# Performance work log

Measured on AMD Instinct MI355X. Metric: run time of the kernel, lower is better.

The kernel has to match this reference:

```python
import jax, jax.numpy as jnp
import numpy as np

BATCH, SEQ, DIM, NH = 2, 4096, 1024, 16
HD = DIM // NH
BLOCK = 64


def setup_inputs() -> dict:
    key = jax.random.key(0)
    ks = jax.random.split(key, 8)
    x = jax.random.normal(ks[0], (BATCH, SEQ, DIM), dtype=jnp.float32)
    # standard RoPE tables: (seq, head_dim)
    inv_freq = 1.0 / (10000.0 ** (jnp.arange(0, HD, 2, dtype=jnp.float32) / HD))
    t = jnp.arange(SEQ, dtype=jnp.float32)
    freqs = jnp.outer(t, inv_freq)                      # (SEQ, HD//2)
    emb = jnp.concatenate([freqs, freqs], axis=-1)      # (SEQ, HD)
    cos, sin = jnp.cos(emb), jnp.sin(emb)
    s = 0.02
    wq = jax.random.normal(ks[1], (DIM, DIM), jnp.float32) * s
    wk = jax.random.normal(ks[2], (DIM, DIM), jnp.float32) * s
    wv = jax.random.normal(ks[3], (DIM, DIM), jnp.float32) * s
    wo = jax.random.normal(ks[4], (DIM, DIM), jnp.float32) * s
    A_log = jax.random.normal(ks[5], (NH,), jnp.float32) * 0.1
    w_dt_w = jax.random.normal(ks[6], (DIM, NH), jnp.float32) * s
    w_dt_b = jnp.zeros((NH,), jnp.float32)
    return {"x": x, "cos": cos, "sin": sin, "wq": wq, "wk": wk, "wv": wv,
            "wo": wo, "A_log": A_log, "w_dt_w": w_dt_w, "w_dt_b": w_dt_b}


def segsum(a):
    """a: (..., T) -> (..., T, T) lower-triangular segment sums, -inf above diag."""
    T = a.shape[-1]
    cs = jnp.cumsum(a, axis=-1)
    seg = cs[..., :, None] - cs[..., None, :]
    mask = jnp.tril(jnp.ones((T, T), dtype=bool))
    return jnp.where(mask, seg, -jnp.inf)


def rotate_half(t):
    t1, t2 = jnp.split(t, 2, axis=-1)
    return jnp.concatenate([-t2, t1], axis=-1)


def ssd(X, A, B, C, block_len):
    """Mamba-2 SSD chunked scan.
    X: (b,l,h,p)  A: (b,l,h)  B,C: (b,l,h,n)
    """
    b, l, h, p = X.shape
    c = l // block_len
    Xc = X.reshape(b, c, block_len, h, p)
    Bc = B.reshape(b, c, block_len, h, -1)
    Cc = C.reshape(b, c, block_len, h, -1)
    Ac = jnp.transpose(A.reshape(b, c, block_len, h), (0, 3, 1, 2))  # (b,h,c,l)
    A_cumsum = jnp.cumsum(Ac, axis=-1)
    # intra-chunk (diagonal block) output
    L = jnp.exp(segsum(Ac))                                          # (b,h,c,l,l)
    Y_diag = jnp.einsum('bclhn,bcshn,bhcls,bcshp->bclhp', Cc, Bc, L, Xc)
    # per-chunk states
    decay_states = jnp.exp(A_cumsum[:, :, :, -1:] - A_cumsum)        # (b,h,c,l)
    states = jnp.einsum('bclhn,bhcl,bclhp->bchpn', Bc, decay_states, Xc)
    init = jnp.zeros_like(states[:, :1])
    states = jnp.concatenate([init, states], axis=1)                 # (b,c+1,h,p,n)
    # inter-chunk recurrence (done as a 1-SS matmul over chunk axis)
    A_last = jnp.pad(A_cumsum[:, :, :, -1], ((0, 0), (0, 0), (1, 0)))
    decay_chunk = jnp.exp(segsum(A_last))                            # (b,h,c+1,c+1)
    new_states = jnp.einsum('bhzc,bchpn->bzhpn', decay_chunk, states)
    states, final_state = new_states[:, :-1], new_states[:, -1]
    # state -> output contribution
    state_decay_out = jnp.exp(A_cumsum)
    Y_off = jnp.einsum('bclhn,bchpn,bhcl->bclhp', Cc, states, state_decay_out)
    Y = (Y_diag + Y_off).reshape(b, l, h, p)
    return Y, final_state


def reference(x, cos, sin, wq, wk, wv, wo, A_log, w_dt_w, w_dt_b):
    b, l, dim = x.shape
    h = A_log.shape[0]
    d = dim // h
    xq = (x @ wq).reshape(b, l, h, d)
    xk = (x @ wk).reshape(b, l, h, d)
    xv = (x @ wv).reshape(b, l, h, d)
    cb = cos[None, :, None, :]
    sb = sin[None, :, None, :]
    xq = xq * cb + rotate_half(xq) * sb
    xk = xk * cb + rotate_half(xk) * sb
    dt = jax.nn.softplus(x @ w_dt_w + w_dt_b)           # (b,l,h)
    A = -jnp.exp(A_log)[None, None, :] * dt             # (b,l,h)
    X = xv * dt[..., None]                              # (b,l,h,d)
    Y, state = ssd(X, A, xk, xq, BLOCK)
    # replicate torch's transpose(1,2).view(b, l, -1) exactly:
    y = jnp.transpose(Y, (0, 2, 1, 3)).reshape(b, l, h * d)
    return y @ wo, state
```

## Files before the change

### kernel.cpp

```cpp
#include <hip/hip_runtime.h>


typedef __bf16 bf16x8 __attribute__((ext_vector_type(8)));
typedef float f32x4 __attribute__((ext_vector_type(4)));
typedef unsigned int u32x4 __attribute__((ext_vector_type(4)));
typedef unsigned short u16x8 __attribute__((ext_vector_type(8)));
typedef unsigned short u16x4 __attribute__((ext_vector_type(4)));

__device__ __forceinline__ unsigned short f2bf(float f) {
  unsigned int u = __builtin_bit_cast(unsigned int, f);
  u += 0x7fffu + ((u >> 16) & 1u);
  return (unsigned short)(u >> 16);
}
__device__ __forceinline__ float bf2f(unsigned short s) {
  unsigned int u = ((unsigned int)s) << 16;
  return __builtin_bit_cast(float, u);
}

#define GLOAD16(gp, lp)                                                \
  __builtin_amdgcn_global_load_lds(                                    \
      (const __attribute__((address_space(1))) void*)(gp),             \
      (__attribute__((address_space(3))) void*)(lp), 16, 0, 0)

__global__ __launch_bounds__(256) void convert_bf16_kernel(
    const float* __restrict__ in, unsigned short* __restrict__ out, int n4,
    const float* __restrict__ wdt, unsigned short* __restrict__ wdt_bf) {
  const int bx = blockIdx.x;
  if (bx < 8192) {
    int g = bx * 256 + threadIdx.x;
    if (g < n4) {
      f32x4 v = *reinterpret_cast<const f32x4*>(in + (size_t)g * 4);
      u16x4 o;
      o.x = f2bf(v.x); o.y = f2bf(v.y); o.z = f2bf(v.z); o.w = f2bf(v.w);
      *reinterpret_cast<u16x4*>(out + (size_t)g * 4) = o;
    }
  } else {
    const int g = (bx - 8192) * 256 + threadIdx.x;
    const int n = g >> 10, k = g & 1023;
    wdt_bf[g] = f2bf(wdt[k * 16 + n]);
  }
}

__global__ __launch_bounds__(256) void transpose_w_kernel(
    const float* __restrict__ w0, const float* __restrict__ w1,
    const float* __restrict__ w2, const float* __restrict__ w3,
    unsigned short* __restrict__ wt) {
  __shared__ float tile[32][33];
  const int z = blockIdx.z;
  const float* w = (z == 0) ? w0 : (z == 1) ? w1 : (z == 2) ? w2 : w3;
  unsigned short* o = wt + (size_t)z * 1024 * 1024;
  const int bx = blockIdx.x, by = blockIdx.y;
  const int tx = threadIdx.x, ty = threadIdx.y;
#pragma unroll
  for (int i = 0; i < 4; ++i)
    tile[ty + i * 8][tx] = w[(size_t)(by * 32 + ty + i * 8) * 1024 + bx * 32 + tx];
  __syncthreads();
#pragma unroll
  for (int i = 0; i < 4; ++i)
    o[(size_t)(bx * 32 + ty + i * 8) * 1024 + by * 32 + tx] = f2bf(tile[tx][ty + i * 8]);
}

__global__ __launch_bounds__(256) void dt_gemm_kernel(
    const unsigned short* __restrict__ A,
    const unsigned short* __restrict__ Bt,
    const float* __restrict__ bdt, float* __restrict__ dt) {
  __shared__ unsigned short As[2 * 64 * 32];
  const int tid = threadIdx.x, lane = tid & 63, w = tid >> 6;
  const int m0 = blockIdx.x * 64;
  const unsigned short* ga =
      A + (size_t)(m0 + w * 16 + (lane >> 2)) * 1024 + (lane & 3) * 8;
  unsigned short* la = As + w * 512;
  const int lr = lane & 15, lk = (lane >> 4) * 8;
  const unsigned short* gb = Bt + (size_t)lr * 1024 + lk;
  f32x4 acc = {};
  for (int kt = 0; kt < 1024; kt += 64) {
    GLOAD16(ga + kt, la);
    GLOAD16(ga + kt + 32, la + 2048);
    bf16x8 bF0 = *reinterpret_cast<const bf16x8*>(gb + kt);
    bf16x8 bF1 = *reinterpret_cast<const bf16x8*>(gb + kt + 32);
    __syncthreads();
    bf16x8 aF0 = *reinterpret_cast<const bf16x8*>(&As[(w * 16 + lr) * 32 + lk]);
    bf16x8 aF1 = *reinterpret_cast<const bf16x8*>(&As[2048 + (w * 16 + lr) * 32 + lk]);
    acc = __builtin_amdgcn_mfma_f32_16x16x32_bf16(aF0, bF0, acc, 0, 0, 0);
    acc = __builtin_amdgcn_mfma_f32_16x16x32_bf16(aF1, bF1, acc, 0, 0, 0);
    __syncthreads();
  }
  const int h = lr;
  const float bv = bdt[h];
#pragma unroll
  for (int r = 0; r < 4; ++r) {
    const int row = m0 + w * 16 + (lane >> 4) * 4 + r;
    const float a = acc[r] + bv;
    const float sp = (a > 0.f) ? (a + log1pf(expf(-a))) : log1pf(expf(a));
    dt[(size_t)row * 16 + h] = sp;
  }
}

template <int EPI>
__global__ __launch_bounds__(256) void gemm128_kernel(
    const unsigned short* __restrict__ A, const unsigned short* __restrict__ Bt,
    void* __restrict__ out0, unsigned short* __restrict__ out1,
    unsigned short* __restrict__ out2, const float* __restrict__ cosb,
    const float* __restrict__ sinb, const float* __restrict__ dtb) {
  __shared__ unsigned short As[128 * 64];
  __shared__ unsigned short Bs[128 * 64];
  const int tid = threadIdx.x, lane = tid & 63, w = tid >> 6;
  const int m0 = blockIdx.y * 128, n0 = blockIdx.x * 128;
  const int rw = lane >> 3;
  const int cu = ((lane & 7) ^ rw) * 8;
  const unsigned short* ga = A + (size_t)(m0 + w * 8 + rw) * 1024 + cu;
  const unsigned short* gb = Bt + (size_t)(n0 + w * 8 + rw) * 1024 + cu;
  unsigned short* la = As + (w * 8) * 64;
  unsigned short* lb = Bs + (w * 8) * 64;
  const int lr = lane & 15, lku = lane >> 4;
  const int wr = w >> 1, wc = w & 1;
  const int xr = lr & 7;
  f32x4 acc[4][4] = {};
  for (int kt = 0; kt < 1024; kt += 64) {
#pragma unroll
    for (int g = 0; g < 4; ++g) {
      GLOAD16(ga + kt + (size_t)(g * 32) * 1024, la + g * 32 * 64);
      GLOAD16(gb + kt + (size_t)(g * 32) * 1024, lb + g * 32 * 64);
    }
    __syncthreads();
#pragma unroll
    for (int kk = 0; kk < 2; ++kk) {
      const int un = (kk * 4 + lku) ^ xr;
      bf16x8 aF[4], bF[4];
#pragma unroll
      for (int i = 0; i < 4; ++i) {
        aF[i] = *reinterpret_cast<const bf16x8*>(&As[(wr * 64 + i * 16 + lr) * 64 + un * 8]);
        bF[i] = *reinterpret_cast<const bf16x8*>(&Bs[(wc * 64 + i * 16 + lr) * 64 + un * 8]);
      }
#pragma unroll
      for (int i = 0; i < 4; ++i)
#pragma unroll
        for (int j = 0; j < 4; ++j)
          acc[i][j] = __builtin_amdgcn_mfma_f32_16x16x32_bf16(aF[i], bF[j], acc[i][j], 0, 0, 0);
    }
    __syncthreads();
  }
  const int r0 = m0 + wr * 64 + ((lane >> 4) << 2);
  if constexpr (EPI == 0) {
    float* O = (float*)out0;
    const int c0 = n0 + wc * 64 + lr;
#pragma unroll
    for (int i = 0; i < 4; ++i)
#pragma unroll
      for (int j = 0; j < 4; ++j)
#pragma unroll
        for (int r = 0; r < 4; ++r)
          O[(size_t)(r0 + i * 16 + r) * 1024 + c0 + j * 16] = acc[i][j][r];
  } else {
    const int col = n0 + wc * 64;
    if (col < 2048) {
      unsigned short* O = (col < 1024) ? (unsigned short*)out0 : out1;
      const int cbase = col & 1023;
#pragma unroll
      for (int i = 0; i < 4; ++i)
#pragma unroll
        for (int jj = 0; jj < 2; ++jj) {
          const int d1 = jj * 16 + lr;
#pragma unroll
          for (int r = 0; r < 4; ++r) {
            const int row = r0 + i * 16 + r;
            const int l = row & 4095;
            const float cv = cosb[(size_t)l * 64 + d1];
            const float sv = sinb[(size_t)l * 64 + d1];
            const float v1 = acc[i][jj][r], v2 = acc[i][jj + 2][r];
            O[(size_t)row * 1024 + cbase + jj * 16 + lr] = f2bf(v1 * cv - v2 * sv);
            O[(size_t)row * 1024 + cbase + jj * 16 + lr + 32] = f2bf(v2 * cv + v1 * sv);
          }
        }
    } else {
      unsigned short* O = out2;
      const int cbase = col - 2048;
      const int h = cbase >> 6;
#pragma unroll
      for (int i = 0; i < 4; ++i)
#pragma unroll
        for (int r = 0; r < 4; ++r) {
          const int row = r0 + i * 16 + r;
          const float dtv = dtb[(size_t)row * 16 + h];
#pragma unroll
          for (int j = 0; j < 4; ++j)
            O[(size_t)row * 1024 + cbase + j * 16 + lr] = f2bf(acc[i][j][r] * dtv);
        }
    }
  }
}

__global__ __launch_bounds__(256) void ssd_states_kernel(
    const unsigned short* __restrict__ Kb, const unsigned short* __restrict__ Xb,
    const float* __restrict__ dtb, const float* __restrict__ A_log,
    unsigned short* __restrict__ chunk_states, float* __restrict__ chunk_dec) {
  __shared__ unsigned short T1[64 * 72], T2[64 * 72];
  __shared__ unsigned short BtL[64 * 72], XdL[64 * 72];
  __shared__ float csL[64], decL[64];
  const int c = blockIdx.x, h = blockIdx.y, b = blockIdx.z;
  const int tid = threadIdx.x, lane = tid & 63, w = tid >> 6;
  const size_t gbase = ((size_t)(b * 4096 + c * 64)) * 1024 + h * 64;
  {
    const int s = tid >> 2, e0 = (tid & 3) * 16;
    const unsigned short* gk = Kb + gbase + (size_t)s * 1024 + e0;
    const unsigned short* gx = Xb + gbase + (size_t)s * 1024 + e0;
    *(u32x4*)&T1[s * 72 + e0] = *(const u32x4*)gk;
    *(u32x4*)&T1[s * 72 + e0 + 8] = *(const u32x4*)(gk + 8);
    *(u32x4*)&T2[s * 72 + e0] = *(const u32x4*)gx;
    *(u32x4*)&T2[s * 72 + e0 + 8] = *(const u32x4*)(gx + 8);
  }
  if (w == 0) {
    float a = -expf(A_log[h]) * dtb[((size_t)(b * 4096 + c * 64 + lane)) * 16 + h];
    float v = a;
#pragma unroll
    for (int d = 1; d < 64; d <<= 1) {
      float o = __shfl_up(v, d, 64);
      if (lane >= d) v += o;
    }
    const float tot = __shfl(v, 63, 64);
    csL[lane] = v;
    decL[lane] = expf(tot - v);
    if (lane == 0) chunk_dec[((size_t)(b * 16 + h)) * 64 + c] = expf(tot);
  }
  __syncthreads();
#pragma unroll
  for (int q = 0; q < 2; ++q) {
    const int p = lane;
    const int s0 = (q * 4 + w) * 8;
    u16x8 vb, vx;
#pragma unroll
    for (int j = 0; j < 8; ++j) {
      vb[j] = T1[(s0 + j) * 72 + p];
      vx[j] = f2bf(bf2f(T2[(s0 + j) * 72 + p]) * decL[s0 + j]);
    }
    *(u16x8*)&BtL[p * 72 + s0] = vb;
    *(u16x8*)&XdL[p * 72 + s0] = vx;
  }
  __syncthreads();
  const int lr = lane & 15, lk = (lane >> 4) * 8;
  f32x4 acc[4] = {};
#pragma unroll
  for (int kt = 0; kt < 64; kt += 32) {
    bf16x8 aF = *reinterpret_cast<const bf16x8*>(&XdL[(w * 16 + lr) * 72 + kt + lk]);
#pragma unroll
    for (int j = 0; j < 4; ++j) {
      bf16x8 bF = *reinterpret_cast<const bf16x8*>(&BtL[(j * 16 + lr) * 72 + kt + lk]);
      acc[j] = __builtin_amdgcn_mfma_f32_16x16x32_bf16(aF, bF, acc[j], 0, 0, 0);
    }
  }
  const size_t stb = ((size_t)((b * 64 + c) * 16 + h)) * 4096;
#pragma unroll
  for (int j = 0; j < 4; ++j)
#pragma unroll
    for (int r = 0; r < 4; ++r)
      chunk_states[stb + (size_t)(w * 16 + (lane >> 4) * 4 + r) * 64 + j * 16 + lr] =
          f2bf(acc[j][r]);
}

__global__ __launch_bounds__(256) void scan_kernel(
    const unsigned short* __restrict__ chunk_states, const float* __restrict__ chunk_dec,
    unsigned short* __restrict__ inc_bf, float* __restrict__ state_out) {
  __shared__ float decs[64];
  const int g = blockIdx.x * 256 + threadIdx.x;
  const int n = g & 63, p = (g >> 6) & 63, h = (g >> 12) & 15, b = g >> 16;
  if (threadIdx.x < 64)
    decs[threadIdx.x] = chunk_dec[(size_t)((blockIdx.x * 256) >> 12 & 15) * 64 +
                                  (size_t)(blockIdx.x >> 8) * 1024 + threadIdx.x];
  __syncthreads();
  const size_t pn = (size_t)p * 64 + n;
  const size_t stride = (size_t)16 * 4096;
  const size_t base0 = ((size_t)(b * 64) * 16 + h) * 4096 + pn;
  float inc = 0.f;
  float cur = bf2f(chunk_states[base0]);
  for (int c = 0; c < 64; ++c) {
    const size_t idx = base0 + (size_t)c * stride;
    inc_bf[idx] = f2bf(inc);
    float nxt = (c < 63) ? bf2f(chunk_states[idx + stride]) : 0.f;
    inc = decs[c] * inc + cur;
    cur = nxt;
  }
  state_out[((size_t)(b * 16 + h) * 64 + p) * 64 + n] = inc;
}

__global__ __launch_bounds__(256) void ssd_y_kernel(
    const unsigned short* __restrict__ Qb, const unsigned short* __restrict__ Kb,
    const unsigned short* __restrict__ Xb, const unsigned short* __restrict__ Sg,
    const float* __restrict__ dtb, const float* __restrict__ A_log,
    unsigned short* __restrict__ y_bf) {
  __shared__ unsigned short Cb[64 * 72], Bb[64 * 72], Sb[64 * 72];
  __shared__ unsigned short Xt[64 * 72], TG[64 * 72];
  __shared__ float csL[64], sdeL[64];
  const int c = blockIdx.x, h = blockIdx.y, b = blockIdx.z;
  const int tid = threadIdx.x, lane = tid & 63, w = tid >> 6;
  const size_t gbase = ((size_t)(b * 4096 + c * 64)) * 1024 + h * 64;
  const size_t sbase = ((size_t)((b * 64 + c) * 16 + h)) * 4096;
  {
    const int s = tid >> 2, e0 = (tid & 3) * 16;
    const unsigned short* gq = Qb + gbase + (size_t)s * 1024 + e0;
    const unsigned short* gk = Kb + gbase + (size_t)s * 1024 + e0;
    const unsigned short* gx = Xb + gbase + (size_t)s * 1024 + e0;
    const unsigned short* gs = Sg + sbase + (size_t)s * 64 + e0;
    *(u32x4*)&Cb[s * 72 + e0] = *(const u32x4*)gq;
    *(u32x4*)&Cb[s * 72 + e0 + 8] = *(const u32x4*)(gq + 8);
    *(u32x4*)&Bb[s * 72 + e0] = *(const u32x4*)gk;
    *(u32x4*)&Bb[s * 72 + e0 + 8] = *(const u32x4*)(gk + 8);
    *(u32x4*)&TG[s * 72 + e0] = *(const u32x4*)gx;
    *(u32x4*)&TG[s * 72 + e0 + 8] = *(const u32x4*)(gx + 8);
    *(u32x4*)&Sb[s * 72 + e0] = *(const u32x4*)gs;
    *(u32x4*)&Sb[s * 72 + e0 + 8] = *(const u32x4*)(gs + 8);
  }
  if (w == 0) {
    float a = -expf(A_log[h]) * dtb[((size_t)(b * 4096 + c * 64 + lane)) * 16 + h];
    float v = a;
#pragma unroll
    for (int d = 1; d < 64; d <<= 1) {
      float o = __shfl_up(v, d, 64);
      if (lane >= d) v += o;
    }
    csL[lane] = v;
    sdeL[lane] = expf(v);
  }
  __syncthreads();
  const int lr = lane & 15, lk = (lane >> 4) * 8;
  f32x4 g[4] = {};
#pragma unroll
  for (int kt = 0; kt < 64; kt += 32) {
    bf16x8 aF = *reinterpret_cast<const bf16x8*>(&Cb[(w * 16 + lr) * 72 + kt + lk]);
#pragma unroll
    for (int j = 0; j < 4; ++j) {
      bf16x8 bF = *reinterpret_cast<const bf16x8*>(&Bb[(j * 16 + lr) * 72 + kt + lk]);
      g[j] = __builtin_amdgcn_mfma_f32_16x16x32_bf16(aF, bF, g[j], 0, 0, 0);
    }
  }
#pragma unroll
  for (int q = 0; q < 2; ++q) {
    const int p = lane;
    const int s0 = (q * 4 + w) * 8;
    u16x8 vx;
#pragma unroll
    for (int j = 0; j < 8; ++j) vx[j] = TG[(s0 + j) * 72 + p];
    *(u16x8*)&Xt[p * 72 + s0] = vx;
  }
  __syncthreads();
#pragma unroll
  for (int j = 0; j < 4; ++j)
#pragma unroll
    for (int r = 0; r < 4; ++r) {
      const int l = w * 16 + (lane >> 4) * 4 + r;
      const int s = j * 16 + lr;
      const float gm = (l >= s) ? g[j][r] * expf(csL[l] - csL[s]) : 0.f;
      TG[l * 72 + s] = f2bf(gm);
    }
  {
    const int rl = tid >> 2, e0 = (tid & 3) * 16;
    const float sde = sdeL[rl];
#pragma unroll
    for (int half = 0; half < 2; ++half) {
      u16x8 v = *(u16x8*)&Cb[rl * 72 + e0 + half * 8];
#pragma unroll
      for (int j = 0; j < 8; ++j) v[j] = f2bf(bf2f(v[j]) * sde);
      *(u16x8*)&Cb[rl * 72 + e0 + half * 8] = v;
    }
  }
  __syncthreads();
  f32x4 acc[4] = {};
#pragma unroll
  for (int kt = 0; kt < 64; kt += 32) {
    bf16x8 aG = *reinterpret_cast<const bf16x8*>(&TG[(w * 16 + lr) * 72 + kt + lk]);
    bf16x8 aC = *reinterpret_cast<const bf16x8*>(&Cb[(w * 16 + lr) * 72 + kt + lk]);
#pragma unroll
    for (int j = 0; j < 4; ++j) {
      bf16x8 bX = *reinterpret_cast<const bf16x8*>(&Xt[(j * 16 + lr) * 72 + kt + lk]);
      bf16x8 bS = *reinterpret_cast<const bf16x8*>(&Sb[(j * 16 + lr) * 72 + kt + lk]);
      acc[j] = __builtin_amdgcn_mfma_f32_16x16x32_bf16(aG, bX, acc[j], 0, 0, 0);
      acc[j] = __builtin_amdgcn_mfma_f32_16x16x32_bf16(aC, bS, acc[j], 0, 0, 0);
    }
  }
  const size_t orow = (size_t)b * 4096 + h * 256 + c * 4 + w;
#pragma unroll
  for (int j = 0; j < 4; ++j)
#pragma unroll
    for (int r = 0; r < 4; ++r) {
      const int li = (lane >> 4) * 4 + r;
      y_bf[orow * 1024 + li * 64 + j * 16 + lr] = f2bf(acc[j][r]);
    }
}

extern "C" void kernel_launch(void* const* d_in, const int* in_sizes, int n_in,
                              void* d_out, int out_size, void* d_ws, size_t ws_size,
                              hipStream_t stream) {
  (void)in_sizes; (void)n_in; (void)out_size; (void)ws_size;
  const float* x = (const float*)d_in[0];
  const float* cosb = (const float*)d_in[1];
  const float* sinb = (const float*)d_in[2];
  const float* wq = (const float*)d_in[3];
  const float* wk = (const float*)d_in[4];
  const float* wv = (const float*)d_in[5];
  const float* wo = (const float*)d_in[6];
  const float* A_log = (const float*)d_in[7];
  const float* wdt = (const float*)d_in[8];
  const float* bdt = (const float*)d_in[9];

  float* out_y = (float*)d_out;
  float* out_state = out_y + 8388608;

  const size_t MBB = 1048576;
  char* ws = (char*)d_ws;
  unsigned short* x_bf = (unsigned short*)(ws);
  unsigned short* w_t = (unsigned short*)(ws + 16 * MBB);
  unsigned short* q_bf = (unsigned short*)(ws + 24 * MBB);
  unsigned short* k_bf = (unsigned short*)(ws + 40 * MBB);
  unsigned short* xv_bf = (unsigned short*)(ws + 56 * MBB);
  float* dtb = (float*)(ws + 72 * MBB);
  unsigned short* wdt_bf = (unsigned short*)(ws + 73 * MBB);
  unsigned short* chunk_states = (unsigned short*)(ws + 74 * MBB);
  float* chunk_dec = (float*)(ws + 90 * MBB);
  unsigned short* inc_bf = (unsigned short*)(ws + 91 * MBB);

  convert_bf16_kernel<<<8256, 256, 0, stream>>>(x, x_bf, 2097152, wdt, wdt_bf);
  transpose_w_kernel<<<dim3(32, 32, 4), dim3(32, 8), 0, stream>>>(wq, wk, wv, wo, w_t);
  dt_gemm_kernel<<<128, 256, 0, stream>>>(x_bf, wdt_bf, bdt, dtb);

  gemm128_kernel<3><<<dim3(24, 64), 256, 0, stream>>>(
      x_bf, w_t, q_bf, k_bf, xv_bf, cosb, sinb, dtb);

  ssd_states_kernel<<<dim3(64, 16, 2), 256, 0, stream>>>(k_bf, xv_bf, dtb, A_log,
                                                         chunk_states, chunk_dec);
  scan_kernel<<<512, 256, 0, stream>>>(chunk_states, chunk_dec, inc_bf, out_state);
  ssd_y_kernel<<<dim3(64, 16, 2), 256, 0, stream>>>(q_bf, k_bf, xv_bf, inc_bf, dtb, A_log,
                                                    x_bf );

  gemm128_kernel<0><<<dim3(8, 64), 256, 0, stream>>>(
      x_bf , w_t + 3 * MBB, out_y, nullptr, nullptr, nullptr, nullptr, nullptr);
}
```

Measured before the change: 162.4 us.

## Use 256x128 GEMM tiles with 512 threads and triple-buffered async LDS loads

Replaces the 128x128 single-buffered GEMM with a 256x128 tile run by 8 waves. It uses a three-stage ring of LDS buffers filled by global_load_lds, with vmcnt-based waits and one barrier per k-step. MFMA blocks are raised with s_setprio. The goal is to overlap global loads with matrix math and raise per-wave reuse, at the cost of much more LDS (144 KB), fewer blocks and a different wave-to-column mapping in the RoPE and dt epilogues.

```diff
diff --git a/kernel.cpp b/kernel.cpp
--- a/kernel.cpp
+++ b/kernel.cpp
@@ -97,94 +97,124 @@
 }
 
 template <int EPI>
-__global__ __launch_bounds__(256) void gemm128_kernel(
+__global__ __launch_bounds__(512, 2) void gemm256_kernel(
     const unsigned short* __restrict__ A, const unsigned short* __restrict__ Bt,
     void* __restrict__ out0, unsigned short* __restrict__ out1,
     unsigned short* __restrict__ out2, const float* __restrict__ cosb,
     const float* __restrict__ sinb, const float* __restrict__ dtb) {
-  __shared__ unsigned short As[128 * 64];
-  __shared__ unsigned short Bs[128 * 64];
+  __shared__ unsigned short AsBuf[3][256 * 64];
+  __shared__ unsigned short BsBuf[3][128 * 64];
   const int tid = threadIdx.x, lane = tid & 63, w = tid >> 6;
-  const int m0 = blockIdx.y * 128, n0 = blockIdx.x * 128;
-  const int rw = lane >> 3;
-  const int cu = ((lane & 7) ^ rw) * 8;
-  const unsigned short* ga = A + (size_t)(m0 + w * 8 + rw) * 1024 + cu;
-  const unsigned short* gb = Bt + (size_t)(n0 + w * 8 + rw) * 1024 + cu;
-  unsigned short* la = As + (w * 8) * 64;
-  unsigned short* lb = Bs + (w * 8) * 64;
-  const int lr = lane & 15, lku = lane >> 4;
-  const int wr = w >> 1, wc = w & 1;
+  const int wr = w >> 2, wc = w & 3;
+  const int m0 = blockIdx.y * 256, n0 = blockIdx.x * 128;
+  const int srw = lane >> 3;
+  const int scu = ((lane & 7) ^ srw) * 8;
+  const unsigned short* gA = A + (size_t)(m0 + w * 32 + srw) * 1024 + scu;
+  const unsigned short* gB = Bt + (size_t)(n0 + w * 16 + srw) * 1024 + scu;
+  const int lr = lane & 15, l4 = lane >> 4;
   const int xr = lr & 7;
-  f32x4 acc[4][4] = {};
-  for (int kt = 0; kt < 1024; kt += 64) {
-#pragma unroll
-    for (int g = 0; g < 4; ++g) {
-      GLOAD16(ga + kt + (size_t)(g * 32) * 1024, la + g * 32 * 64);
-      GLOAD16(gb + kt + (size_t)(g * 32) * 1024, lb + g * 32 * 64);
-    }
-    __syncthreads();
+  f32x4 acc[8][2] = {};
+
+  auto STAGE = [&](unsigned short* as, unsigned short* bs, int kt) {
+#pragma unroll
+    for (int g = 0; g < 4; ++g)
+      GLOAD16(gA + kt + (size_t)(g * 8) * 1024, as + (w * 32 + g * 8) * 64);
+#pragma unroll
+    for (int g = 0; g < 2; ++g)
+      GLOAD16(gB + kt + (size_t)(g * 8) * 1024, bs + (w * 16 + g * 8) * 64);
+  };
+  auto COMPUTE = [&](const unsigned short* as, const unsigned short* bs) {
+    bf16x8 aF[2][8], bF[2][2];
 #pragma unroll
     for (int kk = 0; kk < 2; ++kk) {
-      const int un = (kk * 4 + lku) ^ xr;
-      bf16x8 aF[4], bF[4];
-#pragma unroll
-      for (int i = 0; i < 4; ++i) {
-        aF[i] = *reinterpret_cast<const bf16x8*>(&As[(wr * 64 + i * 16 + lr) * 64 + un * 8]);
-        bF[i] = *reinterpret_cast<const bf16x8*>(&Bs[(wc * 64 + i * 16 + lr) * 64 + un * 8]);
-      }
-#pragma unroll
-      for (int i = 0; i < 4; ++i)
-#pragma unroll
-        for (int j = 0; j < 4; ++j)
-          acc[i][j] = __builtin_amdgcn_mfma_f32_16x16x32_bf16(aF[i], bF[j], acc[i][j], 0, 0, 0);
-    }
-    __syncthreads();
-  }
-  const int r0 = m0 + wr * 64 + ((lane >> 4) << 2);
+      const int un = (((kk * 4 + l4) ^ xr) * 8);
+#pragma unroll
+      for (int i = 0; i < 8; ++i)
+        aF[kk][i] = *reinterpret_cast<const bf16x8*>(
+            &as[(wr * 128 + i * 16 + lr) * 64 + un]);
+#pragma unroll
+      for (int j = 0; j < 2; ++j)
+        bF[kk][j] = *reinterpret_cast<const bf16x8*>(
+            &bs[((wc >> 1) * 64 + (wc & 1) * 16 + j * 32 + lr) * 64 + un]);
+    }
+    __builtin_amdgcn_s_setprio(1);
+#pragma unroll
+    for (int kk = 0; kk < 2; ++kk)
+#pragma unroll
+      for (int i = 0; i < 8; ++i)
+#pragma unroll
+        for (int j = 0; j < 2; ++j)
+          acc[i][j] = __builtin_amdgcn_mfma_f32_16x16x32_bf16(
+              aF[kk][i], bF[kk][j], acc[i][j], 0, 0, 0);
+    __builtin_amdgcn_s_setprio(0);
+  };
+
+  unsigned short *pa0 = AsBuf[0], *pa1 = AsBuf[1], *pa2 = AsBuf[2];
+  unsigned short *pb0 = BsBuf[0], *pb1 = BsBuf[1], *pb2 = BsBuf[2];
+  STAGE(pa0, pb0, 0);
+  STAGE(pa1, pb1, 64);
+  asm volatile("s_waitcnt vmcnt(6)" ::: "memory");
+  __builtin_amdgcn_s_barrier();
+  asm volatile("" ::: "memory");
+  const int NT = 16;
+  for (int t = 0; t < NT; ++t) {
+    if (t < NT - 2) STAGE(pa2, pb2, (t + 2) * 64);
+    COMPUTE(pa0, pb0);
+    if (t < NT - 1) {
+      if (t < NT - 2)
+        asm volatile("s_waitcnt vmcnt(6)" ::: "memory");
+      else
+        asm volatile("s_waitcnt vmcnt(0)" ::: "memory");
+      __builtin_amdgcn_s_barrier();
+      asm volatile("" ::: "memory");
+    }
+    unsigned short* ta = pa0; pa0 = pa1; pa1 = pa2; pa2 = ta;
+    unsigned short* tb = pb0; pb0 = pb1; pb1 = pb2; pb2 = tb;
+  }
+
+  const int rbase = m0 + wr * 128 + l4 * 4;
   if constexpr (EPI == 0) {
     float* O = (float*)out0;
-    const int c0 = n0 + wc * 64 + lr;
-#pragma unroll
-    for (int i = 0; i < 4; ++i)
-#pragma unroll
-      for (int j = 0; j < 4; ++j)
+#pragma unroll
+    for (int i = 0; i < 8; ++i)
+#pragma unroll
+      for (int j = 0; j < 2; ++j) {
+        const int c = n0 + (wc >> 1) * 64 + (wc & 1) * 16 + j * 32 + lr;
 #pragma unroll
         for (int r = 0; r < 4; ++r)
-          O[(size_t)(r0 + i * 16 + r) * 1024 + c0 + j * 16] = acc[i][j][r];
+          O[(size_t)(rbase + i * 16 + r) * 1024 + c] = acc[i][j][r];
+      }
   } else {
-    const int col = n0 + wc * 64;
-    if (col < 2048) {
-      unsigned short* O = (col < 1024) ? (unsigned short*)out0 : out1;
-      const int cbase = col & 1023;
-#pragma unroll
-      for (int i = 0; i < 4; ++i)
-#pragma unroll
-        for (int jj = 0; jj < 2; ++jj) {
-          const int d1 = jj * 16 + lr;
-#pragma unroll
-          for (int r = 0; r < 4; ++r) {
-            const int row = r0 + i * 16 + r;
-            const int l = row & 4095;
-            const float cv = cosb[(size_t)l * 64 + d1];
-            const float sv = sinb[(size_t)l * 64 + d1];
-            const float v1 = acc[i][jj][r], v2 = acc[i][jj + 2][r];
-            O[(size_t)row * 1024 + cbase + jj * 16 + lr] = f2bf(v1 * cv - v2 * sv);
-            O[(size_t)row * 1024 + cbase + jj * 16 + lr + 32] = f2bf(v2 * cv + v1 * sv);
-          }
+    const int colh = n0 + (wc >> 1) * 64;
+    if (colh < 2048) {
+      unsigned short* O = (colh < 1024) ? (unsigned short*)out0 : out1;
+      const int cb = colh & 1023;
+      const int d1 = (wc & 1) * 16 + lr;
+#pragma unroll
+      for (int i = 0; i < 8; ++i)
+#pragma unroll
+        for (int r = 0; r < 4; ++r) {
+          const int row = rbase + i * 16 + r;
+          const int l = row & 4095;
+          const float cv = cosb[(size_t)l * 64 + d1];
+          const float sv = sinb[(size_t)l * 64 + d1];
+          const float v1 = acc[i][0][r], v2 = acc[i][1][r];
+          O[(size_t)row * 1024 + cb + d1] = f2bf(v1 * cv - v2 * sv);
+          O[(size_t)row * 1024 + cb + d1 + 32] = f2bf(v2 * cv + v1 * sv);
         }
     } else {
       unsigned short* O = out2;
-      const int cbase = col - 2048;
-      const int h = cbase >> 6;
-#pragma unroll
-      for (int i = 0; i < 4; ++i)
+      const int h = (colh - 2048) >> 6;
+      const int cb = colh - 2048 + (wc & 1) * 16;
+#pragma unroll
+      for (int i = 0; i < 8; ++i)
 #pragma unroll
         for (int r = 0; r < 4; ++r) {
-          const int row = r0 + i * 16 + r;
+          const int row = rbase + i * 16 + r;
           const float dtv = dtb[(size_t)row * 16 + h];
 #pragma unroll
-          for (int j = 0; j < 4; ++j)
-            O[(size_t)row * 1024 + cbase + j * 16 + lr] = f2bf(acc[i][j][r] * dtv);
+          for (int j = 0; j < 2; ++j)
+            O[(size_t)row * 1024 + cb + j * 32 + lr] = f2bf(acc[i][j][r] * dtv);
         }
     }
   }
@@ -421,7 +451,7 @@
   transpose_w_kernel<<<dim3(32, 32, 4), dim3(32, 8), 0, stream>>>(wq, wk, wv, wo, w_t);
   dt_gemm_kernel<<<128, 256, 0, stream>>>(x_bf, wdt_bf, bdt, dtb);
 
-  gemm128_kernel<3><<<dim3(24, 64), 256, 0, stream>>>(
+  gemm256_kernel<3><<<dim3(24, 32), 512, 0, stream>>>(
       x_bf, w_t, q_bf, k_bf, xv_bf, cosb, sinb, dtb);
 
   ssd_states_kernel<<<dim3(64, 16, 2), 256, 0, stream>>>(k_bf, xv_bf, dtb, A_log,
@@ -430,6 +460,6 @@
   ssd_y_kernel<<<dim3(64, 16, 2), 256, 0, stream>>>(q_bf, k_bf, xv_bf, inc_bf, dtb, A_log,
                                                     x_bf );
 
-  gemm128_kernel<0><<<dim3(8, 64), 256, 0, stream>>>(
+  gemm256_kernel<0><<<dim3(8, 32), 512, 0, stream>>>(
       x_bf , w_t + 3 * MBB, out_y, nullptr, nullptr, nullptr, nullptr, nullptr);
 }
```

After: 178.8 us. 1.1x slower.

## Replace QKV GEMM with 256x256 triple-buffered pipelined 8-wave kernel

Applied to the files above, without the earlier changes.

The fused QKV projection moves from a 128x128 tile with single-buffered LDS and full syncs to a 256x256 tile run by 512 threads. It uses a three-stage LDS ring with global_load_lds prefetch, split barriers, and setprio around the MFMA bursts so loads overlap compute. The larger tile raises reuse per LDS load but halves the K-step to 32 and cuts the grid from 1536 to 384 blocks. That can hurt CU fill on a large GPU and adds register pressure from 32 accumulators. The output projection is split into its own kernel, with no speed change intended there.

```diff
diff --git a/kernel.cpp b/kernel.cpp
--- a/kernel.cpp
+++ b/kernel.cpp
@@ -21,6 +21,13 @@
   __builtin_amdgcn_global_load_lds(                                    \
       (const __attribute__((address_space(1))) void*)(gp),             \
       (__attribute__((address_space(3))) void*)(lp), 16, 0, 0)
+
+#define BARR()                              \
+  do {                                      \
+    asm volatile("" ::: "memory");          \
+    __builtin_amdgcn_s_barrier();           \
+    asm volatile("" ::: "memory");          \
+  } while (0)
 
 __global__ __launch_bounds__(256) void convert_bf16_kernel(
     const float* __restrict__ in, unsigned short* __restrict__ out, int n4,
@@ -96,12 +103,129 @@
   }
 }
 
-template <int EPI>
-__global__ __launch_bounds__(256) void gemm128_kernel(
+__global__ __launch_bounds__(512, 2) void gemm256_qkv_kernel(
     const unsigned short* __restrict__ A, const unsigned short* __restrict__ Bt,
-    void* __restrict__ out0, unsigned short* __restrict__ out1,
-    unsigned short* __restrict__ out2, const float* __restrict__ cosb,
+    unsigned short* __restrict__ oq, unsigned short* __restrict__ ok,
+    unsigned short* __restrict__ ov, const float* __restrict__ cosb,
     const float* __restrict__ sinb, const float* __restrict__ dtb) {
+  __shared__ unsigned short As[3][8192];
+  __shared__ unsigned short Bs[3][8192];
+  const int tid = threadIdx.x, lane = tid & 63, w = tid >> 6;
+  const int wr = w >> 2, wc = w & 3;
+  const int m0 = blockIdx.y * 256, n0 = blockIdx.x * 256;
+  const int srow = lane >> 2;
+  const int sunit = (lane & 3) ^ (srow & 3);
+  const unsigned short* gA = A + (size_t)(m0 + w * 32 + srow) * 1024 + sunit * 8;
+  const unsigned short* gB = Bt + (size_t)(n0 + w * 32 + srow) * 1024 + sunit * 8;
+  const int lr = lane & 15, s4 = lane >> 4;
+  const int un = (s4 ^ (lr & 3)) * 8;
+  f32x4 acc[8][4] = {};
+
+  auto SA = [&](unsigned short* buf, int kt) {
+    GLOAD16(gA + kt, buf + w * 1024);
+    GLOAD16(gA + kt + (size_t)16 * 1024, buf + w * 1024 + 512);
+  };
+  auto SB = [&](unsigned short* buf, int kt) {
+    GLOAD16(gB + kt, buf + w * 1024);
+    GLOAD16(gB + kt + (size_t)16 * 1024, buf + w * 1024 + 512);
+  };
+
+  unsigned short *a0 = As[0], *a1 = As[1], *a2 = As[2];
+  unsigned short *b0 = Bs[0], *b1 = Bs[1], *b2 = Bs[2];
+  SA(a0, 0); SB(b0, 0);
+  SA(a1, 32); SB(b1, 32);
+  asm volatile("s_waitcnt vmcnt(4)" ::: "memory");
+  __builtin_amdgcn_s_barrier();
+
+  for (int t = 0; t < 32; ++t) {
+    const int kt2 = t * 32 + 64;
+    bf16x8 aF[4], bF[4];
+#pragma unroll
+    for (int i = 0; i < 4; ++i)
+      aF[i] = *reinterpret_cast<const bf16x8*>(
+          &a0[(wr * 128 + i * 16 + lr) * 32 + un]);
+#pragma unroll
+    for (int j = 0; j < 4; ++j)
+      bF[j] = *reinterpret_cast<const bf16x8*>(
+          &b0[(wc * 64 + j * 16 + lr) * 32 + un]);
+    if (t < 30) SA(a2, kt2);
+    BARR();
+    __builtin_amdgcn_sched_barrier(0);
+    __builtin_amdgcn_s_setprio(1);
+#pragma unroll
+    for (int i = 0; i < 4; ++i)
+#pragma unroll
+      for (int j = 0; j < 4; ++j)
+        acc[i][j] = __builtin_amdgcn_mfma_f32_16x16x32_bf16(
+            aF[i], bF[j], acc[i][j], 0, 0, 0);
+    __builtin_amdgcn_s_setprio(0);
+    BARR();
+    bf16x8 aG[4];
+#pragma unroll
+    for (int i = 0; i < 4; ++i)
+      aG[i] = *reinterpret_cast<const bf16x8*>(
+          &a0[(wr * 128 + (i + 4) * 16 + lr) * 32 + un]);
+    if (t < 30) SB(b2, kt2);
+    BARR();
+    __builtin_amdgcn_sched_barrier(0);
+    __builtin_amdgcn_s_setprio(1);
+#pragma unroll
+    for (int i = 0; i < 4; ++i)
+#pragma unroll
+      for (int j = 0; j < 4; ++j)
+        acc[i + 4][j] = __builtin_amdgcn_mfma_f32_16x16x32_bf16(
+            aG[i], bF[j], acc[i + 4][j], 0, 0, 0);
+    __builtin_amdgcn_s_setprio(0);
+    if (t < 30)
+      asm volatile("s_waitcnt vmcnt(4)" ::: "memory");
+    else if (t == 30)
+      asm volatile("s_waitcnt vmcnt(0)" ::: "memory");
+    if (t < 31) BARR();
+    unsigned short* ta = a0; a0 = a1; a1 = a2; a2 = ta;
+    unsigned short* tb = b0; b0 = b1; b1 = b2; b2 = tb;
+  }
+
+  const int rbase = m0 + wr * 128 + s4 * 4;
+  const int cblock = n0 + wc * 64;
+  if (cblock < 2048) {
+    unsigned short* O = (cblock < 1024) ? oq : ok;
+    const int cb = cblock & 1023;
+#pragma unroll
+    for (int i = 0; i < 8; ++i)
+#pragma unroll
+      for (int jj = 0; jj < 2; ++jj) {
+        const int d1 = jj * 16 + lr;
+#pragma unroll
+        for (int r = 0; r < 4; ++r) {
+          const int row = rbase + i * 16 + r;
+          const int l = row & 4095;
+          const float cv = cosb[(size_t)l * 64 + d1];
+          const float sv = sinb[(size_t)l * 64 + d1];
+          const float v1 = acc[i][jj][r], v2 = acc[i][jj + 2][r];
+          O[(size_t)row * 1024 + cb + d1] = f2bf(v1 * cv - v2 * sv);
+          O[(size_t)row * 1024 + cb + d1 + 32] = f2bf(v2 * cv + v1 * sv);
+        }
+      }
+  } else {
+    unsigned short* O = ov;
+    const int cb = cblock - 2048;
+    const int h = cb >> 6;
+#pragma unroll
+    for (int i = 0; i < 8; ++i)
+#pragma unroll
+      for (int r = 0; r < 4; ++r) {
+        const int row = rbase + i * 16 + r;
+        const float dtv = dtb[(size_t)row * 16 + h];
+#pragma unroll
+        for (int j = 0; j < 4; ++j)
+          O[(size_t)row * 1024 + cb + j * 16 + lr] = f2bf(acc[i][j][r] * dtv);
+      }
+  }
+}
+
+__global__ __launch_bounds__(256) void gemm128_wo_kernel(
+    const unsigned short* __restrict__ A, const unsigned short* __restrict__ Bt,
+    float* __restrict__ O) {
   __shared__ unsigned short As[128 * 64];
   __shared__ unsigned short Bs[128 * 64];
   const int tid = threadIdx.x, lane = tid & 63, w = tid >> 6;
@@ -125,12 +249,12 @@
     __syncthreads();
 #pragma unroll
     for (int kk = 0; kk < 2; ++kk) {
-      const int un = (kk * 4 + lku) ^ xr;
+      const int un = (((kk * 4 + lku) ^ xr) * 8);
       bf16x8 aF[4], bF[4];
 #pragma unroll
       for (int i = 0; i < 4; ++i) {
-        aF[i] = *reinterpret_cast<const bf16x8*>(&As[(wr * 64 + i * 16 + lr) * 64 + un * 8]);
-        bF[i] = *reinterpret_cast<const bf16x8*>(&Bs[(wc * 64 + i * 16 + lr) * 64 + un * 8]);
+        aF[i] = *reinterpret_cast<const bf16x8*>(&As[(wr * 64 + i * 16 + lr) * 64 + un]);
+        bF[i] = *reinterpret_cast<const bf16x8*>(&Bs[(wc * 64 + i * 16 + lr) * 64 + un]);
       }
 #pragma unroll
       for (int i = 0; i < 4; ++i)
@@ -141,53 +265,14 @@
     __syncthreads();
   }
   const int r0 = m0 + wr * 64 + ((lane >> 4) << 2);
-  if constexpr (EPI == 0) {
-    float* O = (float*)out0;
-    const int c0 = n0 + wc * 64 + lr;
-#pragma unroll
-    for (int i = 0; i < 4; ++i)
-#pragma unroll
-      for (int j = 0; j < 4; ++j)
-#pragma unroll
-        for (int r = 0; r < 4; ++r)
-          O[(size_t)(r0 + i * 16 + r) * 1024 + c0 + j * 16] = acc[i][j][r];
-  } else {
-    const int col = n0 + wc * 64;
-    if (col < 2048) {
-      unsigned short* O = (col < 1024) ? (unsigned short*)out0 : out1;
-      const int cbase = col & 1023;
-#pragma unroll
-      for (int i = 0; i < 4; ++i)
-#pragma unroll
-        for (int jj = 0; jj < 2; ++jj) {
-          const int d1 = jj * 16 + lr;
-#pragma unroll
-          for (int r = 0; r < 4; ++r) {
-            const int row = r0 + i * 16 + r;
-            const int l = row & 4095;
-            const float cv = cosb[(size_t)l * 64 + d1];
-            const float sv = sinb[(size_t)l * 64 + d1];
-            const float v1 = acc[i][jj][r], v2 = acc[i][jj + 2][r];
-            O[(size_t)row * 1024 + cbase + jj * 16 + lr] = f2bf(v1 * cv - v2 * sv);
-            O[(size_t)row * 1024 + cbase + jj * 16 + lr + 32] = f2bf(v2 * cv + v1 * sv);
-          }
-        }
-    } else {
-      unsigned short* O = out2;
-      const int cbase = col - 2048;
-      const int h = cbase >> 6;
-#pragma unroll
-      for (int i = 0; i < 4; ++i)
-#pragma unroll
-        for (int r = 0; r < 4; ++r) {
-          const int row = r0 + i * 16 + r;
-          const float dtv = dtb[(size_t)row * 16 + h];
-#pragma unroll
-          for (int j = 0; j < 4; ++j)
-            O[(size_t)row * 1024 + cbase + j * 16 + lr] = f2bf(acc[i][j][r] * dtv);
-        }
-    }
-  }
+  const int c0 = n0 + wc * 64 + lr;
+#pragma unroll
+  for (int i = 0; i < 4; ++i)
+#pragma unroll
+    for (int j = 0; j < 4; ++j)
+#pragma unroll
+      for (int r = 0; r < 4; ++r)
+        O[(size_t)(r0 + i * 16 + r) * 1024 + c0 + j * 16] = acc[i][j][r];
 }
 
 __global__ __launch_bounds__(256) void ssd_states_kernel(
@@ -421,7 +506,7 @@
   transpose_w_kernel<<<dim3(32, 32, 4), dim3(32, 8), 0, stream>>>(wq, wk, wv, wo, w_t);
   dt_gemm_kernel<<<128, 256, 0, stream>>>(x_bf, wdt_bf, bdt, dtb);
 
-  gemm128_kernel<3><<<dim3(24, 64), 256, 0, stream>>>(
+  gemm256_qkv_kernel<<<dim3(12, 32), 512, 0, stream>>>(
       x_bf, w_t, q_bf, k_bf, xv_bf, cosb, sinb, dtb);
 
   ssd_states_kernel<<<dim3(64, 16, 2), 256, 0, stream>>>(k_bf, xv_bf, dtb, A_log,
@@ -430,6 +515,5 @@
   ssd_y_kernel<<<dim3(64, 16, 2), 256, 0, stream>>>(q_bf, k_bf, xv_bf, inc_bf, dtb, A_log,
                                                     x_bf );
 
-  gemm128_kernel<0><<<dim3(8, 64), 256, 0, stream>>>(
-      x_bf , w_t + 3 * MBB, out_y, nullptr, nullptr, nullptr, nullptr, nullptr);
-}
+  gemm128_wo_kernel<<<dim3(8, 64), 256, 0, stream>>>(x_bf , w_t + 3 * MBB, out_y);
+}
```

Result: slower. 177.7 us (+9.4%).
